# Performance work log

Hardware: AMD Instinct MI355X
Metric: run time of the kernel (lower is better)

## Reference

```python
import jax, jax.numpy as jnp
import numpy as np

B, H, S, D = 2, 16, 2048, 64
N_SINK = 1


def setup_inputs() -> dict:
    key = jax.random.key(0)
    kq, kk, ks = jax.random.split(key, 3)
    q = jax.random.normal(kq, (B, H, S, D), dtype=jnp.float32)
    k = jax.random.normal(kk, (B, H, S, D), dtype=jnp.float32)
    sinks = jax.random.normal(ks, (B, H, S, N_SINK), dtype=jnp.float32)
    return {"q": q, "k": k, "sinks": sinks}


def reference(q, k, sinks):
    # scores: [B,H,S,S] = q @ k^T
    scores = jnp.einsum("bhqd,bhkd->bhqk", q, k)
    # per-key norm ||k||, broadcast over query dim: [B,H,1,S]
    denom = jnp.sqrt(jnp.sum(k * k, axis=-1))[..., None, :]
    w = scores / denom
    # causal: zero (NOT -inf) above the diagonal, faithful to torch.tril
    w = jnp.tril(w)
    # append learned sink logits: [B,H,S,S+N_SINK]
    w = jnp.concatenate([w, sinks], axis=-1)
    return jax.nn.softmax(w, axis=-1)
```

## Files before the change

### kernel.cpp

```cpp
#include <hip/hip_runtime.h>
#include <hip/hip_fp16.h>
#include <math.h>

#define S 2048
#define D 64
#define BH 32
#define TILE 64
#define NT (S / TILE)
#define SP1 (S + 1)

typedef _Float16 f16;
typedef f16 f16x8 __attribute__((ext_vector_type(8)));
typedef f16 f16x4 __attribute__((ext_vector_type(4)));
typedef float f32x4 __attribute__((ext_vector_type(4)));

#define LDS_PITCH 72

__global__ __launch_bounds__(256) void knorm_kernel(const float* __restrict__ k,
                                                    float* __restrict__ rinv) {
    int row  = (blockIdx.x * 256 + threadIdx.x) >> 6;
    int lane = threadIdx.x & 63;
    float v = k[(size_t)row * D + lane];
    float s = v * v;
    #pragma unroll
    for (int off = 32; off; off >>= 1) s += __shfl_xor(s, off);
    if (lane == 0) rinv[row] = 1.0f / sqrtf(s);
}

__global__ __launch_bounds__(256) void fused_kernel(
    const float* __restrict__ q, const float* __restrict__ k,
    const float* __restrict__ sinks, const float* __restrict__ rinv,
    float* __restrict__ out)
{
    __shared__ __align__(16) f16 qs[TILE * LDS_PITCH];
    __shared__ __align__(16) f16 ks[TILE * LDS_PITCH];
    __shared__ float ils[TILE];

    const int it = NT - 1 - blockIdx.x;
    const int bh = blockIdx.y;
    const int i0 = it * TILE;
    const int tid  = threadIdx.x;
    const int lane = tid & 63;
    const int w    = tid >> 6;
    const int m    = lane & 15;
    const int quad = lane >> 4;

    const float* qbase = q + (size_t)bh * S * D;
    const float* kbase = k + (size_t)bh * S * D;
    const float* rbase = rinv + (size_t)bh * S;
    float* obase = out + (size_t)bh * S * SP1;

    {
        int r  = tid >> 4;
        int c4 = (tid & 15) * 4;
        #pragma unroll
        for (int rb = 0; rb < 4; rb++) {
            int row = rb * 16 + r;
            float4 v = *(const float4*)(qbase + (size_t)(i0 + row) * D + c4);
            f16x4 hv; hv[0] = (f16)v.x; hv[1] = (f16)v.y; hv[2] = (f16)v.z; hv[3] = (f16)v.w;
            *(f16x4*)&qs[row * LDS_PITCH + c4] = hv;
        }
    }
    __syncthreads();

    f16x8 a0 = *(const f16x8*)&qs[(w * 16 + m) * LDS_PITCH + 0  + quad * 8];
    f16x8 a1 = *(const f16x8*)&qs[(w * 16 + m) * LDS_PITCH + 32 + quad * 8];

    const int ib = i0 + w * 16 + quad * 4;

    float rowsum[4] = {0.f, 0.f, 0.f, 0.f};
    for (int jt = 0; jt <= it; jt++) {
        const int j0 = jt * TILE;
        __syncthreads();
        {
            int r  = tid >> 4;
            int c4 = (tid & 15) * 4;
            #pragma unroll
            for (int rb = 0; rb < 4; rb++) {
                int row = rb * 16 + r;
                float4 v = *(const float4*)(kbase + (size_t)(j0 + row) * D + c4);
                f16x4 hv; hv[0] = (f16)v.x; hv[1] = (f16)v.y; hv[2] = (f16)v.z; hv[3] = (f16)v.w;
                *(f16x4*)&ks[row * LDS_PITCH + c4] = hv;
            }
        }
        __syncthreads();

        const bool diag = (jt == it);
        #pragma unroll
        for (int st = 0; st < 4; st++) {
            f16x8 b0 = *(const f16x8*)&ks[(st * 16 + m) * LDS_PITCH + 0  + quad * 8];
            f16x8 b1 = *(const f16x8*)&ks[(st * 16 + m) * LDS_PITCH + 32 + quad * 8];
            f32x4 acc = {0.f, 0.f, 0.f, 0.f};
            acc = __builtin_amdgcn_mfma_f32_16x16x32_f16(a0, b0, acc, 0, 0, 0);
            acc = __builtin_amdgcn_mfma_f32_16x16x32_f16(a1, b1, acc, 0, 0, 0);
            const int j = j0 + st * 16 + m;
            const float rj = rbase[j];
            #pragma unroll
            for (int r = 0; r < 4; r++) {
                float e = __expf(acc[r] * rj);
                if (diag && j > ib + r) e = 0.0f;
                rowsum[r] += e;
            }
        }
    }

    #pragma unroll
    for (int off = 1; off < 16; off <<= 1)
        #pragma unroll
        for (int r = 0; r < 4; r++) rowsum[r] += __shfl_xor(rowsum[r], off);

    if (m == 0) {
        #pragma unroll
        for (int r = 0; r < 4; r++) {
            int i = ib + r;
            float l = rowsum[r] + (float)(S - 1 - i) + __expf(sinks[bh * S + i]);
            ils[w * 16 + quad * 4 + r] = 1.0f / l;
        }
    }
    __syncthreads();

    if (tid < TILE) {
        int i = i0 + tid;
        obase[(size_t)i * SP1 + S] = __expf(sinks[bh * S + i]) * ils[tid];
    }

    float il[4];
    #pragma unroll
    for (int r = 0; r < 4; r++) il[r] = ils[w * 16 + quad * 4 + r];

    for (int jt = 0; jt < NT; jt++) {
        const int j0 = jt * TILE;
        if (jt <= it) {
            __syncthreads();
            {
                int r  = tid >> 4;
                int c4 = (tid & 15) * 4;
                #pragma unroll
                for (int rb = 0; rb < 4; rb++) {
                    int row = rb * 16 + r;
                    float4 v = *(const float4*)(kbase + (size_t)(j0 + row) * D + c4);
                    f16x4 hv; hv[0] = (f16)v.x; hv[1] = (f16)v.y; hv[2] = (f16)v.z; hv[3] = (f16)v.w;
                    *(f16x4*)&ks[row * LDS_PITCH + c4] = hv;
                }
            }
            __syncthreads();

            const bool diag = (jt == it);
            #pragma unroll
            for (int st = 0; st < 4; st++) {
                f16x8 b0 = *(const f16x8*)&ks[(st * 16 + m) * LDS_PITCH + 0  + quad * 8];
                f16x8 b1 = *(const f16x8*)&ks[(st * 16 + m) * LDS_PITCH + 32 + quad * 8];
                f32x4 acc = {0.f, 0.f, 0.f, 0.f};
                acc = __builtin_amdgcn_mfma_f32_16x16x32_f16(a0, b0, acc, 0, 0, 0);
                acc = __builtin_amdgcn_mfma_f32_16x16x32_f16(a1, b1, acc, 0, 0, 0);
                const int j = j0 + st * 16 + m;
                const float rj = rbase[j];
                #pragma unroll
                for (int r = 0; r < 4; r++) {
                    float val = __expf(acc[r] * rj) * il[r];
                    if (diag && j > ib + r) val = il[r];
                    obase[(size_t)(ib + r) * SP1 + j] = val;
                }
            }
        } else {
            const int cb = lane;
            #pragma unroll
            for (int r = 0; r < 16; r++) {
                int row = w * 16 + r;
                obase[(size_t)(i0 + row) * SP1 + j0 + cb] = ils[row];
            }
        }
    }
}

extern "C" void kernel_launch(void* const* d_in, const int* in_sizes, int n_in,
                              void* d_out, int out_size, void* d_ws, size_t ws_size,
                              hipStream_t stream) {
    const float* q     = (const float*)d_in[0];
    const float* k     = (const float*)d_in[1];
    const float* sinks = (const float*)d_in[2];
    float* out = (float*)d_out;

    float* rinv = (float*)d_ws;

    knorm_kernel<<<dim3(BH * S / 4), 256, 0, stream>>>(k, rinv);
    fused_kernel<<<dim3(NT, BH), 256, 0, stream>>>(q, k, sinks, rinv, out);
}
```

Before: 723.9 us.

## Double-buffer K tiles with register prefetch and vectorize constant fill stores

K tiles are now double-buffered in LDS, and the next tile is prefetched into registers before the current tile's MFMA work, so each iteration needs one barrier instead of two. The second pass walks tiles in reverse starting from the diagonal, which lets the last K tile of pass one stay resident. The fully masked region is written with 16-byte stores of a packed struct instead of scalar stores. The costs are more LDS and registers, plus unaligned vector stores, since the SP1 row pitch breaks 16-byte alignment.

New measurement: 697.6 us. 1.04x faster.

```diff
diff --git a/kernel.cpp b/kernel.cpp
--- a/kernel.cpp
+++ b/kernel.cpp
@@ -13,6 +13,8 @@
 typedef f16 f16x8 __attribute__((ext_vector_type(8)));
 typedef f16 f16x4 __attribute__((ext_vector_type(4)));
 typedef float f32x4 __attribute__((ext_vector_type(4)));
+
+struct __attribute__((packed, aligned(4))) f4u { float x, y, z, w; };
 
 #define LDS_PITCH 72
 
@@ -33,7 +35,7 @@
     float* __restrict__ out)
 {
     __shared__ __align__(16) f16 qs[TILE * LDS_PITCH];
-    __shared__ __align__(16) f16 ks[TILE * LDS_PITCH];
+    __shared__ __align__(16) f16 ks[2][TILE * LDS_PITCH];
     __shared__ float ils[TILE];
 
     const int it = NT - 1 - blockIdx.x;
@@ -44,23 +46,42 @@
     const int w    = tid >> 6;
     const int m    = lane & 15;
     const int quad = lane >> 4;
+    const int sr   = tid >> 4;
+    const int sc4  = (tid & 15) * 4;
 
     const float* qbase = q + (size_t)bh * S * D;
     const float* kbase = k + (size_t)bh * S * D;
     const float* rbase = rinv + (size_t)bh * S;
     float* obase = out + (size_t)bh * S * SP1;
 
-    {
-        int r  = tid >> 4;
-        int c4 = (tid & 15) * 4;
+    float4 pre[4];
+
+    auto loadk = [&](int jt) {
+        const float* tb = kbase + (size_t)(jt * TILE) * D;
+        #pragma unroll
+        for (int rb = 0; rb < 4; rb++)
+            pre[rb] = *(const float4*)(tb + (size_t)(rb * 16 + sr) * D + sc4);
+    };
+    auto writek = [&](int buf) {
         #pragma unroll
         for (int rb = 0; rb < 4; rb++) {
-            int row = rb * 16 + r;
-            float4 v = *(const float4*)(qbase + (size_t)(i0 + row) * D + c4);
+            float4 v = pre[rb];
             f16x4 hv; hv[0] = (f16)v.x; hv[1] = (f16)v.y; hv[2] = (f16)v.z; hv[3] = (f16)v.w;
-            *(f16x4*)&qs[row * LDS_PITCH + c4] = hv;
+            *(f16x4*)&ks[buf][(rb * 16 + sr) * LDS_PITCH + sc4] = hv;
+        }
+    };
+
+    loadk(0);
+    {
+        #pragma unroll
+        for (int rb = 0; rb < 4; rb++) {
+            int row = rb * 16 + sr;
+            float4 v = *(const float4*)(qbase + (size_t)(i0 + row) * D + sc4);
+            f16x4 hv; hv[0] = (f16)v.x; hv[1] = (f16)v.y; hv[2] = (f16)v.z; hv[3] = (f16)v.w;
+            *(f16x4*)&qs[row * LDS_PITCH + sc4] = hv;
         }
     }
+    writek(0);
     __syncthreads();
 
     f16x8 a0 = *(const f16x8*)&qs[(w * 16 + m) * LDS_PITCH + 0  + quad * 8];
@@ -70,26 +91,14 @@
 
     float rowsum[4] = {0.f, 0.f, 0.f, 0.f};
     for (int jt = 0; jt <= it; jt++) {
+        if (jt < it) loadk(jt + 1);
+        const int buf = jt & 1;
+        const bool diag = (jt == it);
         const int j0 = jt * TILE;
-        __syncthreads();
-        {
-            int r  = tid >> 4;
-            int c4 = (tid & 15) * 4;
-            #pragma unroll
-            for (int rb = 0; rb < 4; rb++) {
-                int row = rb * 16 + r;
-                float4 v = *(const float4*)(kbase + (size_t)(j0 + row) * D + c4);
-                f16x4 hv; hv[0] = (f16)v.x; hv[1] = (f16)v.y; hv[2] = (f16)v.z; hv[3] = (f16)v.w;
-                *(f16x4*)&ks[row * LDS_PITCH + c4] = hv;
-            }
-        }
-        __syncthreads();
-
-        const bool diag = (jt == it);
         #pragma unroll
         for (int st = 0; st < 4; st++) {
-            f16x8 b0 = *(const f16x8*)&ks[(st * 16 + m) * LDS_PITCH + 0  + quad * 8];
-            f16x8 b1 = *(const f16x8*)&ks[(st * 16 + m) * LDS_PITCH + 32 + quad * 8];
+            f16x8 b0 = *(const f16x8*)&ks[buf][(st * 16 + m) * LDS_PITCH + 0  + quad * 8];
+            f16x8 b1 = *(const f16x8*)&ks[buf][(st * 16 + m) * LDS_PITCH + 32 + quad * 8];
             f32x4 acc = {0.f, 0.f, 0.f, 0.f};
             acc = __builtin_amdgcn_mfma_f32_16x16x32_f16(a0, b0, acc, 0, 0, 0);
             acc = __builtin_amdgcn_mfma_f32_16x16x32_f16(a1, b1, acc, 0, 0, 0);
@@ -102,6 +111,8 @@
                 rowsum[r] += e;
             }
         }
+        if (jt < it) writek((jt + 1) & 1);
+        __syncthreads();
     }
 
     #pragma unroll
@@ -128,47 +139,39 @@
     #pragma unroll
     for (int r = 0; r < 4; r++) il[r] = ils[w * 16 + quad * 4 + r];
 
-    for (int jt = 0; jt < NT; jt++) {
+    for (int jt = it; jt >= 0; jt--) {
+        if (jt > 0) loadk(jt - 1);
+        const int buf = jt & 1;
+        const bool diag = (jt == it);
         const int j0 = jt * TILE;
-        if (jt <= it) {
-            __syncthreads();
-            {
-                int r  = tid >> 4;
-                int c4 = (tid & 15) * 4;
-                #pragma unroll
-                for (int rb = 0; rb < 4; rb++) {
-                    int row = rb * 16 + r;
-                    float4 v = *(const float4*)(kbase + (size_t)(j0 + row) * D + c4);
-                    f16x4 hv; hv[0] = (f16)v.x; hv[1] = (f16)v.y; hv[2] = (f16)v.z; hv[3] = (f16)v.w;
-                    *(f16x4*)&ks[row * LDS_PITCH + c4] = hv;
-                }
+        #pragma unroll
+        for (int st = 0; st < 4; st++) {
+            f16x8 b0 = *(const f16x8*)&ks[buf][(st * 16 + m) * LDS_PITCH + 0  + quad * 8];
+            f16x8 b1 = *(const f16x8*)&ks[buf][(st * 16 + m) * LDS_PITCH + 32 + quad * 8];
+            f32x4 acc = {0.f, 0.f, 0.f, 0.f};
+            acc = __builtin_amdgcn_mfma_f32_16x16x32_f16(a0, b0, acc, 0, 0, 0);
+            acc = __builtin_amdgcn_mfma_f32_16x16x32_f16(a1, b1, acc, 0, 0, 0);
+            const int j = j0 + st * 16 + m;
+            const float rj = rbase[j];
+            #pragma unroll
+            for (int r = 0; r < 4; r++) {
+                float val = __expf(acc[r] * rj) * il[r];
+                if (diag && j > ib + r) val = il[r];
+                obase[(size_t)(ib + r) * SP1 + j] = val;
             }
-            __syncthreads();
+        }
+        if (jt > 0) writek((jt - 1) & 1);
+        __syncthreads();
+    }
 
-            const bool diag = (jt == it);
-            #pragma unroll
-            for (int st = 0; st < 4; st++) {
-                f16x8 b0 = *(const f16x8*)&ks[(st * 16 + m) * LDS_PITCH + 0  + quad * 8];
-                f16x8 b1 = *(const f16x8*)&ks[(st * 16 + m) * LDS_PITCH + 32 + quad * 8];
-                f32x4 acc = {0.f, 0.f, 0.f, 0.f};
-                acc = __builtin_amdgcn_mfma_f32_16x16x32_f16(a0, b0, acc, 0, 0, 0);
-                acc = __builtin_amdgcn_mfma_f32_16x16x32_f16(a1, b1, acc, 0, 0, 0);
-                const int j = j0 + st * 16 + m;
-                const float rj = rbase[j];
-                #pragma unroll
-                for (int r = 0; r < 4; r++) {
-                    float val = __expf(acc[r] * rj) * il[r];
-                    if (diag && j > ib + r) val = il[r];
-                    obase[(size_t)(ib + r) * SP1 + j] = val;
-                }
-            }
-        } else {
-            const int cb = lane;
-            #pragma unroll
-            for (int r = 0; r < 16; r++) {
-                int row = w * 16 + r;
-                obase[(size_t)(i0 + row) * SP1 + j0 + cb] = ils[row];
-            }
+    for (int jt = it + 1; jt < NT; jt++) {
+        const int j0 = jt * TILE;
+        #pragma unroll
+        for (int rb = 0; rb < 4; rb++) {
+            int row = w * 16 + rb * 4 + (lane >> 4);
+            float v = ils[row];
+            f4u vv = {v, v, v, v};
+            *(f4u*)&obase[(size_t)(i0 + row) * SP1 + j0 + (lane & 15) * 4] = vv;
         }
     }
 }
```
